# Kernel optimization log

Measured on AMD Instinct MI355X. Metric: run time of the kernel, lower is better.

## Reference

```python
import jax, jax.numpy as jnp
import numpy as np
import math

INPUT_SIZE = 1024
HIDDEN_SIZE = 1024
BATCH = 4096


def setup_inputs() -> dict:
    key = jax.random.key(0)
    ks = jax.random.split(key, 16)
    stddev = 1.0 / math.sqrt(HIDDEN_SIZE)

    def unif(k, shape):
        return jax.random.uniform(k, shape, minval=-stddev, maxval=stddev, dtype=jnp.float32)

    inp = {
        'x': jax.random.normal(ks[0], (BATCH, INPUT_SIZE), dtype=jnp.float32),
        'h_prev': jax.random.normal(ks[1], (BATCH, HIDDEN_SIZE), dtype=jnp.float32),
        'c_prev': jax.random.normal(ks[2], (BATCH, HIDDEN_SIZE), dtype=jnp.float32),
        'igx': unif(ks[3], (INPUT_SIZE, HIDDEN_SIZE)),
        'igu': unif(ks[4], (HIDDEN_SIZE, HIDDEN_SIZE)),
        'ib': unif(ks[5], (HIDDEN_SIZE,)),
        'fgx': unif(ks[6], (INPUT_SIZE, HIDDEN_SIZE)),
        'fgu': unif(ks[7], (HIDDEN_SIZE, HIDDEN_SIZE)),
        'fb': unif(ks[8], (HIDDEN_SIZE,)),
        'ogx': unif(ks[9], (INPUT_SIZE, HIDDEN_SIZE)),
        'ogu': unif(ks[10], (HIDDEN_SIZE, HIDDEN_SIZE)),
        'ob': unif(ks[11], (HIDDEN_SIZE,)),
        'cgx': unif(ks[12], (INPUT_SIZE, HIDDEN_SIZE)),
        'cgu': unif(ks[13], (HIDDEN_SIZE, HIDDEN_SIZE)),
        'cb': unif(ks[14], (HIDDEN_SIZE,)),
    }
    return inp


def reference(x, h_prev, c_prev, igx, igu, ib, fgx, fgu, fb, ogx, ogu, ob, cgx, cgu, cb):
    # Fuse the 8 gate matmuls into 2 GEMMs via concatenated weights.
    # Wx: [input_size, 4H], Wh: [hidden, 4H], b: [4H]; gate order i,f,o,c.
    Wx = jnp.concatenate([igx, fgx, ogx, cgx], axis=1)
    Wh = jnp.concatenate([igu, fgu, ogu, cgu], axis=1)
    b = jnp.concatenate([ib, fb, ob, cb], axis=0)
    gates = x @ Wx + h_prev @ Wh + b  # [B, 4H]
    H = c_prev.shape[-1]
    ig = jax.nn.sigmoid(gates[:, 0 * H:1 * H])
    fg = jax.nn.sigmoid(gates[:, 1 * H:2 * H])
    og = jax.nn.sigmoid(gates[:, 2 * H:3 * H])
    cc = jnp.tanh(gates[:, 3 * H:4 * H])
    c = fg * c_prev + ig * cc
    h = og * jnp.tanh(c)
    return (h, c)
```

## Files before the change

kernel.cpp:

```cpp
#include <hip/hip_runtime.h>
#include <hip/hip_bf16.h>

typedef unsigned short u16;
typedef unsigned int u32;
typedef short bf16x8 __attribute__((ext_vector_type(8)));
typedef float f32x4 __attribute__((ext_vector_type(4)));
typedef u16 u16x8 __attribute__((ext_vector_type(8)));

#define HID 1024
#define BATCH 4096
#define KTOT 2048
#define NT 32
#define A0B 0
#define B0B 16384
#define A1B 32768
#define B1B 49152

__device__ __forceinline__ u16 f2bf(float f) {
  u32 v = __builtin_bit_cast(u32, f);
  u32 r = (v + 0x7fffu + ((v >> 16) & 1u)) >> 16;
  return (u16)r;
}
__device__ __forceinline__ float sigmoid_fast(float x) {
  return 1.0f / (1.0f + __expf(-x));
}
__device__ __forceinline__ float tanh_fast(float x) {
  return 2.0f * sigmoid_fast(2.0f * x) - 1.0f;
}
__device__ __forceinline__ void gl_lds16(const void* g, void* l) {
  __builtin_amdgcn_global_load_lds(
      (const __attribute__((address_space(1))) u32*)g,
      (__attribute__((address_space(3))) u32*)l, 16, 0, 0);
}

__global__ __launch_bounds__(256) void prep_all(
    const float* __restrict__ x, const float* __restrict__ hp,
    const float* __restrict__ igx, const float* __restrict__ fgx,
    const float* __restrict__ ogx, const float* __restrict__ cgx,
    const float* __restrict__ igu, const float* __restrict__ fgu,
    const float* __restrict__ ogu, const float* __restrict__ cgu,
    u16* __restrict__ xh, u16* __restrict__ bt) {
  __shared__ u16 lds[64 * 66];
  if (blockIdx.x < 4096) {
    int c = blockIdx.x * 256 + threadIdx.x;
    int row = c >> 8;
    int col0 = (c & 255) << 3;
    const float* src = (col0 < 1024)
                           ? (x + (size_t)row * 1024 + col0)
                           : (hp + (size_t)row * 1024 + (col0 - 1024));
    f32x4 a = *(const f32x4*)(src);
    f32x4 b = *(const f32x4*)(src + 4);
    u16x8 v;
#pragma unroll
    for (int j = 0; j < 4; ++j) { v[j] = f2bf(a[j]); v[j + 4] = f2bf(b[j]); }
    *(u16x8*)(xh + (size_t)row * KTOT + col0) = v;
    return;
  }
  const float* srcs[8] = {igx, fgx, ogx, cgx, igu, fgu, ogu, cgu};
  int bid = blockIdx.x - 4096;
  int m = bid >> 8;
  int tile = bid & 255;
  int th = tile & 15, tk = tile >> 4;
  int h0 = th << 6, k0 = tk << 6;
  int g = m & 3, which = m >> 2;
  const float* W = srcs[m] + (size_t)k0 * HID + h0;

  int t = threadIdx.x;
  int r1 = t >> 4;
  int c1 = (t & 15) << 2;
#pragma unroll
  for (int p = 0; p < 4; ++p) {
    int row = (p << 4) + r1;
    f32x4 v = *(const f32x4*)(W + (size_t)row * HID + c1);
    u32 p0 = (u32)f2bf(v[0]) | ((u32)f2bf(v[1]) << 16);
    u32 p1 = (u32)f2bf(v[2]) | ((u32)f2bf(v[3]) << 16);
    u32* d = (u32*)&lds[row * 66 + c1];
    d[0] = p0;
    d[1] = p1;
  }
  __syncthreads();
  int nl = t >> 2;
  int kc = t & 3;
  int row_np = ((h0 >> 4) << 6) + ((nl >> 4) << 6) + (g << 4) + (nl & 15);
  size_t dst = (size_t)row_np * KTOT + (size_t)which * 1024 + k0;
  u16x8 a2, b2;
#pragma unroll
  for (int j = 0; j < 8; ++j) {
    a2[j] = lds[(kc * 8 + j) * 66 + nl];
    b2[j] = lds[(kc * 8 + 32 + j) * 66 + nl];
  }
  *(u16x8*)(&bt[dst + kc * 8]) = a2;
  *(u16x8*)(&bt[dst + kc * 8 + 32]) = b2;
}

__global__ __launch_bounds__(512, 2) void lstm_gemm(
    const u16* __restrict__ xh, const u16* __restrict__ bt,
    const float* __restrict__ cprev,
    const float* __restrict__ ib, const float* __restrict__ fb,
    const float* __restrict__ ob, const float* __restrict__ cb,
    float* __restrict__ hout, float* __restrict__ cout) {
  __shared__ __align__(16) u16 lds[4 * 16384];

  int sx = threadIdx.x;
  int bid = blockIdx.x;
  int xcd = bid & 7, lid = bid >> 3;
  int brow = ((xcd & 3) << 2) | (lid & 3);
  int bcol = ((xcd >> 2) << 3) | (lid >> 2);

  int w = sx >> 6, l = sx & 63;
  int wr = (w >> 2) << 7;
  int wc = (w & 3) << 6;
  int lrow = l & 15, q = l >> 4;
  int grow = brow << 8;

  int prow = sx >> 3;
  int koff = ((sx & 7) ^ (prow & 7)) << 3;
  const u16* aS0 = xh + (size_t)(grow + prow) * KTOT + koff;
  const u16* aS1 = aS0 + (size_t)128 * KTOT;
  const u16* bS0 = bt + (size_t)(bcol * 256 + prow) * KTOT + koff;
  const u16* bS1 = bS0 + (size_t)128 * KTOT;
  int sx8 = sx * 8;

  int aoff = (wr + lrow) << 6;
  int boff = (wc + lrow) << 6;
  int pc0 = (q ^ (lrow & 7)) << 3;
  int pc1 = ((q + 4) ^ (lrow & 7)) << 3;

  f32x4 acc[8][4] = {};
  bf16x8 af[2][2], bfr[4][2];

#define STG(P_, K_, D_)                                                       \
  gl_lds16((P_) + (K_), &lds[(D_) + sx8]);                                    \
  gl_lds16((P_) + (size_t)64 * KTOT + (K_), &lds[(D_) + 4096 + sx8]);

  STG(bS0, 0, B0B)
  STG(bS1, 0, B0B + 8192)
  STG(aS0, 0, A0B)
  STG(aS1, 0, A0B + 8192)
  STG(bS0, 64, B1B)
  STG(bS1, 64, B1B + 8192)
  asm volatile("s_waitcnt vmcnt(4)");
  __builtin_amdgcn_s_barrier();
  __builtin_amdgcn_sched_barrier(0);

#define RDA(AB_, i, pc) (*(const bf16x8*)&lds[(AB_) + aoff + (i) * 1024 + (pc)])
#define RDB(BB_, j, pc) (*(const bf16x8*)&lds[(BB_) + boff + (j) * 1024 + (pc)])

#define DO_PHASE(K_, AB_, BB_, STG_STMT_)                                     \
  {                                                                           \
    af[0][0] = RDA(AB_, 2 * (K_), pc0);                                       \
    af[0][1] = RDA(AB_, 2 * (K_), pc1);                                       \
    af[1][0] = RDA(AB_, 2 * (K_) + 1, pc0);                                   \
    af[1][1] = RDA(AB_, 2 * (K_) + 1, pc1);                                   \
    if ((K_) == 0) {                                                          \
      bfr[0][0] = RDB(BB_, 0, pc0); bfr[0][1] = RDB(BB_, 0, pc1);             \
      bfr[1][0] = RDB(BB_, 1, pc0); bfr[1][1] = RDB(BB_, 1, pc1);             \
      bfr[2][0] = RDB(BB_, 2, pc0); bfr[2][1] = RDB(BB_, 2, pc1);             \
      bfr[3][0] = RDB(BB_, 3, pc0); bfr[3][1] = RDB(BB_, 3, pc1);             \
    }                                                                         \
    STG_STMT_                                                                 \
    __builtin_amdgcn_s_barrier();                                             \
    asm volatile("s_waitcnt lgkmcnt(0)");                                     \
    __builtin_amdgcn_sched_barrier(0);                                        \
    __builtin_amdgcn_s_setprio(1);                                            \
    _Pragma("unroll") for (int s2 = 0; s2 < 2; ++s2) {                        \
      _Pragma("unroll") for (int j = 0; j < 4; ++j) {                         \
        acc[2 * (K_)][j] = __builtin_amdgcn_mfma_f32_16x16x32_bf16(           \
            af[0][s2], bfr[j][s2], acc[2 * (K_)][j], 0, 0, 0);                \
        acc[2 * (K_) + 1][j] = __builtin_amdgcn_mfma_f32_16x16x32_bf16(       \
            af[1][s2], bfr[j][s2], acc[2 * (K_) + 1][j], 0, 0, 0);            \
      }                                                                       \
    }                                                                         \
    __builtin_amdgcn_s_setprio(0);                                            \
    __builtin_amdgcn_sched_barrier(0);                                        \
  }

#define BAR() __builtin_amdgcn_s_barrier();
#define BOUND(N_)                                                             \
  asm volatile("s_waitcnt vmcnt(" #N_ ")");                                   \
  __builtin_amdgcn_sched_barrier(0);                                          \
  __builtin_amdgcn_s_barrier();

  for (int tp = 0; tp < 15; ++tp) {
    int t = 2 * tp;
    int kA = (t + 1) << 6;
    int kB = (t + 2) << 6;
    int kA2 = kB;
    int kB2 = (t + 3) << 6;
    DO_PHASE(0, A0B, B0B, STG(aS0, kA, A1B))
    BAR()
    DO_PHASE(1, A0B, B0B, STG(aS1, kA, A1B + 8192))
    BAR()
    DO_PHASE(2, A0B, B0B, STG(bS0, kB, B0B))
    BAR()
    DO_PHASE(3, A0B, B0B, STG(bS1, kB, B0B + 8192))
    BOUND(4)
    DO_PHASE(0, A1B, B1B, STG(aS0, kA2, A0B))
    BAR()
    DO_PHASE(1, A1B, B1B, STG(aS1, kA2, A0B + 8192))
    BAR()
    DO_PHASE(2, A1B, B1B, STG(bS0, kB2, B1B))
    BAR()
    DO_PHASE(3, A1B, B1B, STG(bS1, kB2, B1B + 8192))
    BOUND(4)
  }

  {
    const int kA = 31 << 6;
    DO_PHASE(0, A0B, B0B, STG(aS0, kA, A1B))
    BAR()
    DO_PHASE(1, A0B, B0B, STG(aS1, kA, A1B + 8192))
    BAR()
    DO_PHASE(2, A0B, B0B, )
    BAR()
    DO_PHASE(3, A0B, B0B, )
    BOUND(0)
    DO_PHASE(0, A1B, B1B, )
    BAR()
    DO_PHASE(1, A1B, B1B, )
    BAR()
    DO_PHASE(2, A1B, B1B, )
    BAR()
    DO_PHASE(3, A1B, B1B, )
  }
#undef DO_PHASE
#undef RDA
#undef RDB
#undef STG
#undef BAR
#undef BOUND

  int sb = (bcol << 2) + (w & 3);
  int hcol = (sb << 4) + lrow;
  float bi = ib[hcol];
  float bff = fb[hcol];
  float bo = ob[hcol];
  float bc = cb[hcol];

#pragma unroll
  for (int i = 0; i < 8; ++i) {
    int row0 = grow + wr + i * 16 + q * 4;
#pragma unroll
    for (int r = 0; r < 4; ++r) {
      size_t idx = (size_t)(row0 + r) * HID + hcol;
      float gi = sigmoid_fast(acc[i][0][r] + bi);
      float gf = sigmoid_fast(acc[i][1][r] + bff);
      float go = sigmoid_fast(acc[i][2][r] + bo);
      float gc = tanh_fast(acc[i][3][r] + bc);
      float cp = cprev[idx];
      float cv = gf * cp + gi * gc;
      hout[idx] = go * tanh_fast(cv);
      cout[idx] = cv;
    }
  }
}

extern "C" void kernel_launch(void* const* d_in, const int* in_sizes, int n_in,
                              void* d_out, int out_size, void* d_ws, size_t ws_size,
                              hipStream_t stream) {
  const float* x   = (const float*)d_in[0];
  const float* hp  = (const float*)d_in[1];
  const float* cp  = (const float*)d_in[2];
  const float* igx = (const float*)d_in[3];
  const float* igu = (const float*)d_in[4];
  const float* ib  = (const float*)d_in[5];
  const float* fgx = (const float*)d_in[6];
  const float* fgu = (const float*)d_in[7];
  const float* fb  = (const float*)d_in[8];
  const float* ogx = (const float*)d_in[9];
  const float* ogu = (const float*)d_in[10];
  const float* ob  = (const float*)d_in[11];
  const float* cgx = (const float*)d_in[12];
  const float* cgu = (const float*)d_in[13];
  const float* cb  = (const float*)d_in[14];

  u16* bt = (u16*)d_ws;
  u16* xh = bt + (size_t)4096 * 2048;
  float* hout = (float*)d_out;
  float* cout = hout + (size_t)BATCH * HID;

  prep_all<<<6144, 256, 0, stream>>>(x, hp, igx, fgx, ogx, cgx,
                                     igu, fgu, ogu, cgu, xh, bt);
  lstm_gemm<<<256, 512, 0, stream>>>(xh, bt, cp, ib, fb, ob, cb,
                                     hout, cout);
}
```

Measured before the change: 205.9 us.

## Double-buffer LDS fragment registers to prefetch next phase reads during MFMA

Splits the A and B fragment registers into ping-pong sets so that the LDS reads for the next phase are issued before the current phase's MFMAs, instead of reading and then waiting right before each MFMA group. The B fragments for the next K tile are prefetched in phase 3, and vmcnt waits are reshuffled so that global-to-LDS staging of the next tile completes before those early reads. The goal is to hide LDS read latency behind matrix work. The cost is higher VGPR pressure from the doubled fragment buffers, plus more delicate barrier and waitcnt ordering.

```diff
diff --git a/kernel.cpp b/kernel.cpp
--- a/kernel.cpp
+++ b/kernel.cpp
@@ -127,11 +127,56 @@
   int pc1 = ((q + 4) ^ (lrow & 7)) << 3;
 
   f32x4 acc[8][4] = {};
-  bf16x8 af[2][2], bfr[4][2];
+  bf16x8 afP[2][2], afQ[2][2];
+  bf16x8 bfP[4][2], bfQ[4][2];
 
 #define STG(P_, K_, D_)                                                       \
   gl_lds16((P_) + (K_), &lds[(D_) + sx8]);                                    \
   gl_lds16((P_) + (size_t)64 * KTOT + (K_), &lds[(D_) + 4096 + sx8]);
+
+#define RDA(AB_, i, pc) (*(const bf16x8*)&lds[(AB_) + aoff + (i) * 1024 + (pc)])
+#define RDB(BB_, j, pc) (*(const bf16x8*)&lds[(BB_) + boff + (j) * 1024 + (pc)])
+
+#define ISS_A(D_, AB_, I0_)                                                   \
+  D_[0][0] = RDA(AB_, I0_, pc0);                                              \
+  D_[0][1] = RDA(AB_, I0_, pc1);                                              \
+  D_[1][0] = RDA(AB_, (I0_) + 1, pc0);                                        \
+  D_[1][1] = RDA(AB_, (I0_) + 1, pc1);
+
+#define ISS_B(D_, BB_)                                                        \
+  D_[0][0] = RDB(BB_, 0, pc0); D_[0][1] = RDB(BB_, 0, pc1);                   \
+  D_[1][0] = RDB(BB_, 1, pc0); D_[1][1] = RDB(BB_, 1, pc1);                   \
+  D_[2][0] = RDB(BB_, 2, pc0); D_[2][1] = RDB(BB_, 2, pc1);                   \
+  D_[3][0] = RDB(BB_, 3, pc0); D_[3][1] = RDB(BB_, 3, pc1);
+
+#define MFMA16(K_, AF_, BF_)                                                  \
+  __builtin_amdgcn_s_setprio(1);                                              \
+  _Pragma("unroll") for (int s2 = 0; s2 < 2; ++s2) {                          \
+    _Pragma("unroll") for (int j = 0; j < 4; ++j) {                           \
+      acc[2 * (K_)][j] = __builtin_amdgcn_mfma_f32_16x16x32_bf16(             \
+          AF_[0][s2], BF_[j][s2], acc[2 * (K_)][j], 0, 0, 0);                 \
+      acc[2 * (K_) + 1][j] = __builtin_amdgcn_mfma_f32_16x16x32_bf16(         \
+          AF_[1][s2], BF_[j][s2], acc[2 * (K_) + 1][j], 0, 0, 0);             \
+    }                                                                         \
+  }                                                                           \
+  __builtin_amdgcn_s_setprio(0);                                              \
+  __builtin_amdgcn_sched_barrier(0);
+
+#define DO_PHASE(K_, AF_, BF_, ISSUE_, STG_)                                  \
+  {                                                                           \
+    STG_                                                                      \
+    __builtin_amdgcn_s_barrier();                                             \
+    asm volatile("s_waitcnt lgkmcnt(0)");                                     \
+    __builtin_amdgcn_sched_barrier(0);                                        \
+    ISSUE_                                                                    \
+    __builtin_amdgcn_sched_barrier(0);                                        \
+    MFMA16(K_, AF_, BF_)                                                      \
+  }
+
+#define BAR() __builtin_amdgcn_s_barrier();
+#define VMW(N_)                                                               \
+  asm volatile("s_waitcnt vmcnt(" #N_ ")");                                   \
+  __builtin_amdgcn_sched_barrier(0);
 
   STG(bS0, 0, B0B)
   STG(bS1, 0, B0B + 8192)
@@ -139,96 +184,77 @@
   STG(aS1, 0, A0B + 8192)
   STG(bS0, 64, B1B)
   STG(bS1, 64, B1B + 8192)
-  asm volatile("s_waitcnt vmcnt(4)");
+  VMW(4)
   __builtin_amdgcn_s_barrier();
-  __builtin_amdgcn_sched_barrier(0);
-
-#define RDA(AB_, i, pc) (*(const bf16x8*)&lds[(AB_) + aoff + (i) * 1024 + (pc)])
-#define RDB(BB_, j, pc) (*(const bf16x8*)&lds[(BB_) + boff + (j) * 1024 + (pc)])
-
-#define DO_PHASE(K_, AB_, BB_, STG_STMT_)                                     \
-  {                                                                           \
-    af[0][0] = RDA(AB_, 2 * (K_), pc0);                                       \
-    af[0][1] = RDA(AB_, 2 * (K_), pc1);                                       \
-    af[1][0] = RDA(AB_, 2 * (K_) + 1, pc0);                                   \
-    af[1][1] = RDA(AB_, 2 * (K_) + 1, pc1);                                   \
-    if ((K_) == 0) {                                                          \
-      bfr[0][0] = RDB(BB_, 0, pc0); bfr[0][1] = RDB(BB_, 0, pc1);             \
-      bfr[1][0] = RDB(BB_, 1, pc0); bfr[1][1] = RDB(BB_, 1, pc1);             \
-      bfr[2][0] = RDB(BB_, 2, pc0); bfr[2][1] = RDB(BB_, 2, pc1);             \
-      bfr[3][0] = RDB(BB_, 3, pc0); bfr[3][1] = RDB(BB_, 3, pc1);             \
-    }                                                                         \
-    STG_STMT_                                                                 \
-    __builtin_amdgcn_s_barrier();                                             \
-    asm volatile("s_waitcnt lgkmcnt(0)");                                     \
-    __builtin_amdgcn_sched_barrier(0);                                        \
-    __builtin_amdgcn_s_setprio(1);                                            \
-    _Pragma("unroll") for (int s2 = 0; s2 < 2; ++s2) {                        \
-      _Pragma("unroll") for (int j = 0; j < 4; ++j) {                         \
-        acc[2 * (K_)][j] = __builtin_amdgcn_mfma_f32_16x16x32_bf16(           \
-            af[0][s2], bfr[j][s2], acc[2 * (K_)][j], 0, 0, 0);                \
-        acc[2 * (K_) + 1][j] = __builtin_amdgcn_mfma_f32_16x16x32_bf16(       \
-            af[1][s2], bfr[j][s2], acc[2 * (K_) + 1][j], 0, 0, 0);            \
-      }                                                                       \
-    }                                                                         \
-    __builtin_amdgcn_s_setprio(0);                                            \
-    __builtin_amdgcn_sched_barrier(0);                                        \
-  }
-
-#define BAR() __builtin_amdgcn_s_barrier();
-#define BOUND(N_)                                                             \
-  asm volatile("s_waitcnt vmcnt(" #N_ ")");                                   \
-  __builtin_amdgcn_sched_barrier(0);                                          \
-  __builtin_amdgcn_s_barrier();
+  ISS_B(bfP, B0B)
+  ISS_A(afP, A0B, 0)
+  __builtin_amdgcn_sched_barrier(0);
+
+#define TILE_EVEN(kA_, kB_)                                                   \
+  DO_PHASE(0, afP, bfP, ISS_A(afQ, A0B, 2), STG(aS0, kA_, A1B))               \
+  BAR()                                                                       \
+  DO_PHASE(1, afQ, bfP, ISS_A(afP, A0B, 4), STG(aS1, kA_, A1B + 8192))        \
+  BAR()                                                                       \
+  DO_PHASE(2, afP, bfP, ISS_A(afQ, A0B, 6), STG(bS0, kB_, B0B))               \
+  VMW(6) BAR()                                                                \
+  DO_PHASE(3, afQ, bfP, ISS_B(bfQ, B1B), STG(bS1, kB_, B0B + 8192))           \
+  VMW(4) BAR()                                                                \
+  ISS_A(afP, A1B, 0)                                                          \
+  __builtin_amdgcn_sched_barrier(0);
+
+#define TILE_ODD(kA_, kB_)                                                    \
+  DO_PHASE(0, afP, bfQ, ISS_A(afQ, A1B, 2), STG(aS0, kA_, A0B))               \
+  BAR()                                                                       \
+  DO_PHASE(1, afQ, bfQ, ISS_A(afP, A1B, 4), STG(aS1, kA_, A0B + 8192))        \
+  BAR()                                                                       \
+  DO_PHASE(2, afP, bfQ, ISS_A(afQ, A1B, 6), STG(bS0, kB_, B1B))               \
+  VMW(6) BAR()                                                                \
+  DO_PHASE(3, afQ, bfQ, ISS_B(bfP, B0B), STG(bS1, kB_, B1B + 8192))           \
+  VMW(4) BAR()                                                                \
+  ISS_A(afP, A0B, 0)                                                          \
+  __builtin_amdgcn_sched_barrier(0);
 
   for (int tp = 0; tp < 15; ++tp) {
     int t = 2 * tp;
     int kA = (t + 1) << 6;
     int kB = (t + 2) << 6;
-    int kA2 = kB;
+    int kA2 = (t + 2) << 6;
     int kB2 = (t + 3) << 6;
-    DO_PHASE(0, A0B, B0B, STG(aS0, kA, A1B))
-    BAR()
-    DO_PHASE(1, A0B, B0B, STG(aS1, kA, A1B + 8192))
-    BAR()
-    DO_PHASE(2, A0B, B0B, STG(bS0, kB, B0B))
-    BAR()
-    DO_PHASE(3, A0B, B0B, STG(bS1, kB, B0B + 8192))
-    BOUND(4)
-    DO_PHASE(0, A1B, B1B, STG(aS0, kA2, A0B))
-    BAR()
-    DO_PHASE(1, A1B, B1B, STG(aS1, kA2, A0B + 8192))
-    BAR()
-    DO_PHASE(2, A1B, B1B, STG(bS0, kB2, B1B))
-    BAR()
-    DO_PHASE(3, A1B, B1B, STG(bS1, kB2, B1B + 8192))
-    BOUND(4)
+    TILE_EVEN(kA, kB)
+    TILE_ODD(kA2, kB2)
   }
 
   {
     const int kA = 31 << 6;
-    DO_PHASE(0, A0B, B0B, STG(aS0, kA, A1B))
-    BAR()
-    DO_PHASE(1, A0B, B0B, STG(aS1, kA, A1B + 8192))
-    BAR()
-    DO_PHASE(2, A0B, B0B, )
-    BAR()
-    DO_PHASE(3, A0B, B0B, )
-    BOUND(0)
-    DO_PHASE(0, A1B, B1B, )
-    BAR()
-    DO_PHASE(1, A1B, B1B, )
-    BAR()
-    DO_PHASE(2, A1B, B1B, )
-    BAR()
-    DO_PHASE(3, A1B, B1B, )
+    DO_PHASE(0, afP, bfP, ISS_A(afQ, A0B, 2), STG(aS0, kA, A1B))
+    BAR()
+    DO_PHASE(1, afQ, bfP, ISS_A(afP, A0B, 4), STG(aS1, kA, A1B + 8192))
+    BAR()
+    DO_PHASE(2, afP, bfP, ISS_A(afQ, A0B, 6), )
+    VMW(4) BAR()
+    DO_PHASE(3, afQ, bfP, ISS_B(bfQ, B1B), )
+    VMW(0) BAR()
+    ISS_A(afP, A1B, 0)
+    __builtin_amdgcn_sched_barrier(0);
+    DO_PHASE(0, afP, bfQ, ISS_A(afQ, A1B, 2), )
+    BAR()
+    DO_PHASE(1, afQ, bfQ, ISS_A(afP, A1B, 4), )
+    BAR()
+    DO_PHASE(2, afP, bfQ, ISS_A(afQ, A1B, 6), )
+    BAR()
+    DO_PHASE(3, afQ, bfQ, , )
   }
 #undef DO_PHASE
+#undef MFMA16
+#undef ISS_A
+#undef ISS_B
 #undef RDA
 #undef RDB
 #undef STG
 #undef BAR
-#undef BOUND
+#undef VMW
+#undef TILE_EVEN
+#undef TILE_ODD
 
   int sb = (bcol << 2) + (w & 3);
   int hcol = (sb << 4) + lrow;
```

Measured after the change: 205.6 us. About the same (-0.1%).
